# Optimization experiments

Measured on AMD Instinct MI355X. Metric: run time of the kernel, lower is better.

Reference implementation:

```python
import jax, jax.numpy as jnp
import numpy as np

N = 16383        # complete binary tree, 14 levels
D_NODE = 512
D_SSM = 512
D_STATE = 16
MAX_DEPTH = 14   # number of BFS levels (depth 0..13)
LN_EPS = 1e-5


def setup_inputs() -> dict:
    key = jax.random.key(0)
    ks = jax.random.split(key, 8)
    # tree structure: parent[i] = (i-1)//2, root has parent -1; BFS order == index order
    parent = np.concatenate([np.array([-1]), (np.arange(1, N) - 1) // 2]).astype(np.int64)
    depth = np.floor(np.log2(np.arange(N) + 1)).astype(np.int32)
    s = jax.random.normal(ks[0], (N, D_NODE), jnp.float32)
    w = jax.random.uniform(ks[1], (N,), jnp.float32, minval=0.01, maxval=1.0)
    # parameters (xavier-ish scales)
    W_in = jax.random.normal(ks[2], (D_SSM, D_NODE + 1), jnp.float32) * (1.0 / np.sqrt(D_NODE + 1))
    b_in = jnp.zeros((D_SSM,), jnp.float32)
    W_delta = jax.random.normal(ks[3], (D_SSM, D_SSM), jnp.float32) * (1.0 / np.sqrt(D_SSM))
    # dt-style bias init: softplus(b) ~ dt in [1e-3, 1e-1]
    dt = jnp.exp(jax.random.uniform(ks[4], (D_SSM,), jnp.float32) * (np.log(0.1) - np.log(0.001)) + np.log(0.001))
    b_delta = dt + jnp.log(-jnp.expm1(-dt))
    W_w = jax.random.normal(ks[5], (D_SSM, 1), jnp.float32)
    b_w = jnp.zeros((D_SSM,), jnp.float32)
    A_log = jnp.log(jnp.broadcast_to(jnp.arange(1.0, D_STATE + 1.0, dtype=jnp.float32)[None, :], (D_SSM, D_STATE)))
    D = jnp.ones((D_SSM,), jnp.float32)
    W_B = jax.random.normal(ks[6], (D_STATE, D_SSM), jnp.float32) * (1.0 / np.sqrt(D_SSM))
    b_B = jnp.zeros((D_STATE,), jnp.float32)
    W_C = jax.random.normal(ks[7], (D_STATE, D_SSM), jnp.float32) * (1.0 / np.sqrt(D_SSM))
    b_C = jnp.zeros((D_STATE,), jnp.float32)
    gamma = jnp.ones((D_SSM,), jnp.float32)
    beta = jnp.zeros((D_SSM,), jnp.float32)
    return {"s": s, "w": w, "parent": jnp.asarray(parent), "depth": jnp.asarray(depth),
            "W_in": W_in, "b_in": b_in, "W_delta": W_delta, "b_delta": b_delta,
            "W_w": W_w, "b_w": b_w, "A_log": A_log, "D": D,
            "W_B": W_B, "b_B": b_B, "W_C": W_C, "b_C": b_C,
            "gamma": gamma, "beta": beta}


def reference(s, w, parent, depth, W_in, b_in, W_delta, b_delta, W_w, b_w,
              A_log, D, W_B, b_B, W_C, b_C, gamma, beta):
    n = s.shape[0]
    log_w = jnp.log(w + 1e-6)[:, None]                       # [N, 1]
    feat = jnp.concatenate([s, log_w], axis=1)               # [N, d_node+1]
    x = feat @ W_in.T + b_in                                 # [N, d_ssm]
    delta = jax.nn.softplus(x @ W_delta.T + b_delta) * jax.nn.sigmoid(log_w @ W_w.T + b_w)  # [N, d_ssm]
    A = -jnp.exp(A_log)                                      # [d_ssm, d_state]
    B = x @ W_B.T + b_B                                      # [N, d_state]
    C = x @ W_C.T + b_C                                      # [N, d_state]
    A_bar = jnp.exp(delta[:, :, None] * A[None])             # [N, d_ssm, d_state]
    Bx = (delta * x)[:, :, None] * B[:, None, :]             # [N, d_ssm, d_state]
    # level-parallel tree scan: all nodes at BFS depth l updated together
    par = jnp.maximum(parent, 0)
    has_par = (parent >= 0)[:, None, None]
    H = jnp.zeros((n, A_bar.shape[1], A_bar.shape[2]), x.dtype)
    for lvl in range(MAX_DEPTH):
        h_par = jnp.where(has_par, jnp.take(H, par, axis=0), 0.0)
        H = jnp.where((depth == lvl)[:, None, None], A_bar * h_par + Bx, H)
    Y = jnp.einsum('nds,ns->nd', H, C) + D * x               # [N, d_ssm]
    mu = jnp.mean(Y, axis=-1, keepdims=True)
    var = jnp.var(Y, axis=-1, keepdims=True)
    return (Y - mu) / jnp.sqrt(var + LN_EPS) * gamma + beta
```

## Files before the change

### kernel.cpp

```cpp
#include <hip/hip_runtime.h>
#include <hip/hip_bf16.h>
#include <math.h>

#define D_SSM 512
#define D_STATE 16
#define CKPT_BASE 511
#define N_CKPT 512
#define MPAD 16384

typedef __attribute__((ext_vector_type(8))) short short8;
typedef __attribute__((ext_vector_type(4))) float floatx4;

__device__ __forceinline__ unsigned short f2bf(float f) {
    unsigned int u = __float_as_uint(f);
    unsigned int r = (u + 0x7fffu + ((u >> 16) & 1u)) >> 16;
    return (unsigned short)r;
}
__device__ __forceinline__ float bf2f(unsigned short u) {
    return __uint_as_float(((unsigned int)u) << 16);
}
__device__ __forceinline__ void g2lds16(const void* g, void* l) {
    __builtin_amdgcn_global_load_lds(
        (const __attribute__((address_space(1))) void*)g,
        (__attribute__((address_space(3))) void*)l, 16, 0, 0);
}

__device__ __forceinline__ void pw_powers(float r, float* p) {
    float r2 = r * r, r4 = r2 * r2, r8 = r4 * r4;
    p[0] = r;          p[1] = r2;         p[2] = r2 * r;     p[3] = r4;
    p[4] = r4 * r;     p[5] = r4 * r2;    p[6] = r4 * p[2];  p[7] = r8;
    p[8] = r8 * r;     p[9] = r8 * r2;    p[10] = r8 * p[2]; p[11] = r8 * r4;
    p[12] = r8 * p[4]; p[13] = r8 * p[5]; p[14] = r8 * p[6]; p[15] = r8 * r8;
}

__global__ __launch_bounds__(256) void prep_kernel(
    const float* __restrict__ s, const float* __restrict__ w,
    const float* __restrict__ W_in, const float* __restrict__ W_delta,
    const float* __restrict__ W_B, const float* __restrict__ W_C,
    const float* __restrict__ A_log,
    unsigned short* __restrict__ s_bf, float* __restrict__ lw,
    unsigned short* __restrict__ Win_bf, unsigned short* __restrict__ Wd_bf,
    float* __restrict__ As_tab, int* __restrict__ fast_tab,
    int Nn)
{
    const int b = blockIdx.x, t = threadIdx.x;
    if (b < MPAD) {
        unsigned int pack = 0;
        if (b < Nn) {
            float2 sv = *(const float2*)(s + (size_t)b * 512 + t * 2);
            pack = (unsigned int)f2bf(sv.x) | ((unsigned int)f2bf(sv.y) << 16);
        }
        *(unsigned int*)(s_bf + (size_t)b * 512 + t * 2) = pack;
        if (t == 0) lw[b] = (b < Nn) ? logf(w[b] + 1e-6f) : 0.f;
    } else if (b < MPAD + 512) {
        int c = b - MPAD;
        float a0 = W_in[(size_t)c * 513 + t * 2];
        float a1 = W_in[(size_t)c * 513 + t * 2 + 1];
        *(unsigned int*)(Win_bf + (size_t)c * 512 + t * 2) =
            (unsigned int)f2bf(a0) | ((unsigned int)f2bf(a1) << 16);
    } else if (b < MPAD + 1024) {
        int c = b - MPAD - 512;
        float2 wv = *(const float2*)(W_delta + (size_t)c * 512 + t * 2);
        *(unsigned int*)(Wd_bf + (size_t)c * 512 + t * 2) =
            (unsigned int)f2bf(wv.x) | ((unsigned int)f2bf(wv.y) << 16);
    } else if (b < MPAD + 1024 + 128) {
        int c = b - MPAD - 1024;
        float2 wv; wv.x = 0.f; wv.y = 0.f;
        if (c < 16)      wv = *(const float2*)(W_B + (size_t)c * 512 + t * 2);
        else if (c < 32) wv = *(const float2*)(W_C + (size_t)(c - 16) * 512 + t * 2);
        *(unsigned int*)(Wd_bf + (size_t)(512 + c) * 512 + t * 2) =
            (unsigned int)f2bf(wv.x) | ((unsigned int)f2bf(wv.y) << 16);
    } else {
        int ch = (b - (MPAD + 1024 + 128)) * 256 + t;
        float As0 = -__expf(A_log[ch * 16]);
        bool ok = true;
        #pragma unroll
        for (int q = 1; q < 16; q++) {
            float As = -__expf(A_log[ch * 16 + q]);
            ok = ok && (fabsf(As - (float)(q + 1) * As0) <= 1e-4f * (float)(q + 1));
        }
        As_tab[ch] = As0;
        fast_tab[ch] = ok ? 1 : 0;
    }
}

__global__ __launch_bounds__(256) void gemm_mfma(
    const unsigned short* __restrict__ Abf,
    const unsigned short* __restrict__ Wbf,
    float* __restrict__ outf,
    unsigned short* __restrict__ outbf,
    const float* __restrict__ bias,
    const float* __restrict__ lw,
    const float* __restrict__ wcol, int wcol_stride,
    const float* __restrict__ bw,
    const float* __restrict__ b_B, const float* __restrict__ b_C,
    float* __restrict__ Bm, float* __restrict__ Cm,
    int mode)
{
    __shared__ __align__(16) short As[2][128 * 32];
    __shared__ __align__(16) short Bs[2][128 * 32];
    const int tid = threadIdx.x;
    const int wave = tid >> 6, lane = tid & 63;

    const int nwg  = gridDim.x * gridDim.y;
    const int orig = blockIdx.y * gridDim.x + blockIdx.x;
    const int wsw  = (orig & 7) * (nwg >> 3) + (orig >> 3);
    const int bx   = wsw % gridDim.x;
    const int by   = wsw / gridDim.x;
    const int row0 = by * 128;
    const int col0 = bx * 128;

    const int wr = (wave >> 1) * 64;
    const int wc = (wave & 1) * 64;

    floatx4 acc[4][4] = {};

    const int srow = lane >> 2;
    const int sg   = (lane & 3) ^ ((srow >> 1) & 3);
    const int scol = sg * 8;

    const unsigned short* Ag = Abf + (size_t)(row0 + wave * 16 + srow) * 512 + scol;
    const unsigned short* Wg = Wbf + (size_t)(col0 + wave * 16 + srow) * 512 + scol;
    char* Al = (char*)&As[0][0] + wave * 1024;
    char* Bl = (char*)&Bs[0][0] + wave * 1024;

    #define STAGE(buf, k0)                                              \
        do {                                                            \
            g2lds16(Ag + (k0),            Al + (buf) * 8192);           \
            g2lds16(Ag + 64 * 512 + (k0), Al + (buf) * 8192 + 4096);    \
            g2lds16(Wg + (k0),            Bl + (buf) * 8192);           \
            g2lds16(Wg + 64 * 512 + (k0), Bl + (buf) * 8192 + 4096);    \
        } while (0)

    STAGE(0, 0);
    __syncthreads();

    for (int it = 0; it < 16; ++it) {
        const int cur = it & 1;
        if (it < 15) STAGE(cur ^ 1, (it + 1) * 32);

        short8 af[4], bfr[4];
        #pragma unroll
        for (int i = 0; i < 4; i++) {
            int m = wr + i * 16 + (lane & 15);
            int gm = (lane >> 4) ^ ((m >> 1) & 3);
            af[i] = *(const short8*)&As[cur][m * 32 + gm * 8];
        }
        #pragma unroll
        for (int j = 0; j < 4; j++) {
            int n = wc + j * 16 + (lane & 15);
            int gn = (lane >> 4) ^ ((n >> 1) & 3);
            bfr[j] = *(const short8*)&Bs[cur][n * 32 + gn * 8];
        }
        #pragma unroll
        for (int i = 0; i < 4; i++)
            #pragma unroll
            for (int j = 0; j < 4; j++)
                acc[i][j] = __builtin_amdgcn_mfma_f32_16x16x32_bf16(af[i], bfr[j], acc[i][j], 0, 0, 0);
        __syncthreads();
    }
    #undef STAGE

    if (col0 >= 512) {
        #pragma unroll
        for (int i = 0; i < 4; i++) {
            #pragma unroll
            for (int reg = 0; reg < 4; reg++) {
                int r = row0 + wr + i * 16 + (lane >> 4) * 4 + reg;
                #pragma unroll
                for (int j = 0; j < 4; j++) {
                    int c2 = wc + j * 16 + (lane & 15);
                    float z = acc[i][j][reg];
                    if (c2 < 16)      Bm[(size_t)r * 16 + c2]        = z + b_B[c2];
                    else if (c2 < 32) Cm[(size_t)r * 16 + (c2 - 16)] = z + b_C[c2 - 16];
                }
            }
        }
        return;
    }

    #pragma unroll
    for (int i = 0; i < 4; i++) {
        #pragma unroll
        for (int reg = 0; reg < 4; reg++) {
            int r = row0 + wr + i * 16 + (lane >> 4) * 4 + reg;
            float lwr = lw[r];
            #pragma unroll
            for (int j = 0; j < 4; j++) {
                int c = col0 + wc + j * 16 + (lane & 15);
                float z = acc[i][j][reg] + bias[c];
                if (mode == 0) {
                    float o = z + lwr * wcol[(size_t)c * wcol_stride];
                    outbf[(size_t)r * 512 + c] = f2bf(o);
                } else {
                    float sp = (z > 15.f) ? z : __logf(1.f + __expf(z));
                    float sg2 = __builtin_amdgcn_rcpf(1.f + __expf(-(lwr * wcol[c] + bw[c])));
                    outf[(size_t)r * 512 + c] = sp * sg2;
                }
            }
        }
    }
}

__global__ __launch_bounds__(512, 4) void scan_fused(
    const unsigned short* __restrict__ x_bf, const float* __restrict__ delta,
    const float* __restrict__ Bm, const float* __restrict__ Cm,
    const float* __restrict__ A_log, const float* __restrict__ Dv,
    const float* __restrict__ gamma, const float* __restrict__ beta,
    const float* __restrict__ As_tab, const int* __restrict__ fast_tab,
    float* __restrict__ out)
{
    __shared__ __align__(16) float SMEM[16 * 512 + 31 * 32 + 10 * 16];
    __shared__ int nid[16];
    const int bid = blockIdx.x;
    const int d = threadIdx.x;

    const float As0 = As_tab[d];
    const bool fast = fast_tab[d] != 0;
    const float dvd = Dv[d];

    if (bid < N_CKPT) {
        const int a9 = CKPT_BASE + bid;
        float* const Yb   = SMEM;
        float* const BCs  = SMEM + 8192;
        float* const Banc = SMEM + 8192 + 992;

        for (int idx = d; idx < 31 * 32; idx += 512) {
            int i = idx >> 5, c = idx & 31;
            int v = i + 1;
            int j = 31 - __builtin_clz((unsigned)v);
            int node = ((a9 + 1) << j) - 1 + (v - (1 << j));
            BCs[i * 32 + c] = (c < 16) ? Bm[(size_t)node * 16 + c]
                                       : Cm[(size_t)node * 16 + (c - 16)];
        }
        if (d < 160) {
            int k = d >> 4, ss = d & 15;
            int a = a9;
            for (int q = 0; q < k; q++) a = (a - 1) >> 1;
            Banc[k * 16 + ss] = Bm[(size_t)a * 16 + ss];
        }

        float adl[10]; unsigned short axr[10];
        {
            int a = a9;
            #pragma unroll
            for (int k = 0; k < 10; k++) {
                adl[k] = delta[(size_t)a * 512 + d];
                axr[k] = x_bf[(size_t)a * 512 + d];
                a = (a - 1) >> 1;
            }
        }

        const int n10a = 2 * a9 + 1, n10b = 2 * a9 + 2;
        float pdl[2][7]; unsigned short pxr[2][7]; int pid[2][7];
        auto pf7 = [&](int n11, float* dl, unsigned short* xr, int* id) {
            id[0] = n11;          id[1] = 2 * n11 + 1; id[2] = 2 * id[1] + 1;
            id[3] = id[2] + 1;    id[4] = 2 * n11 + 2; id[5] = 2 * id[4] + 1;
            id[6] = id[5] + 1;
            #pragma unroll
            for (int q = 0; q < 7; q++) {
                dl[q] = delta[(size_t)id[q] * 512 + d];
                xr[q] = x_bf[(size_t)id[q] * 512 + d];
            }
        };
        float d10a = delta[(size_t)n10a * 512 + d];
        unsigned short x10a = x_bf[(size_t)n10a * 512 + d];
        pf7(2 * n10a + 1, pdl[0], pxr[0], pid[0]);

        __syncthreads();

        float H9v[16];
        #pragma unroll
        for (int ss = 0; ss < 16; ss++) H9v[ss] = 0.f;
        {
            float cum = 0.f;
            #pragma unroll
            for (int k = 0; k < 10; k++) {
                float da = adl[k];
                float bx = da * bf2f(axr[k]);
                if (fast) {
                    float r = __expf(As0 * cum);
                    float pw[16]; pw_powers(r, pw);
                    const floatx4* B4 = (const floatx4*)&Banc[k * 16];
                    #pragma unroll
                    for (int q = 0; q < 4; q++) {
                        floatx4 b = B4[q];
                        #pragma unroll
                        for (int u = 0; u < 4; u++) {
                            int ss = q * 4 + u;
                            H9v[ss] = fmaf(bx * pw[ss], b[u], H9v[ss]);
                        }
                    }
                } else {
                    #pragma unroll
                    for (int ss = 0; ss < 16; ss++) {
                        float As = -__expf(A_log[d * 16 + ss]);
                        H9v[ss] = fmaf(bx * __expf(As * cum), Banc[k * 16 + ss], H9v[ss]);
                    }
                }
                cum += da;
            }
        }

        auto step_pf = [&](int bfs, float dlt, unsigned short xraw,
                           const float* Hp, float* Hc, int slot, int n) {
            float xv = bf2f(xraw);
            float bx = dlt * xv;
            float y0 = 0.f, y1 = 0.f;
            const floatx4* B4 = (const floatx4*)&BCs[bfs * 32];
            const floatx4* C4 = (const floatx4*)&BCs[bfs * 32 + 16];
            if (fast) {
                float r = __expf(As0 * dlt);
                float pw[16]; pw_powers(r, pw);
                #pragma unroll
                for (int q = 0; q < 4; q++) {
                    floatx4 b = B4[q], c = C4[q];
                    #pragma unroll
                    for (int u = 0; u < 4; u++) {
                        int ss = q * 4 + u;
                        Hc[ss] = fmaf(pw[ss], Hp[ss], bx * b[u]);
                        if (ss & 1) y1 = fmaf(c[u], Hc[ss], y1);
                        else        y0 = fmaf(c[u], Hc[ss], y0);
                    }
                }
            } else {
                #pragma unroll
                for (int ss = 0; ss < 16; ss++) {
                    float Ab = __expf(dlt * (-__expf(A_log[d * 16 + ss])));
                    Hc[ss] = fmaf(Ab, Hp[ss], bx * BCs[bfs * 32 + ss]);
                    float cc = BCs[bfs * 32 + 16 + ss];
                    if (ss & 1) y1 = fmaf(cc, Hc[ss], y1);
                    else        y0 = fmaf(cc, Hc[ss], y0);
                }
            }
            Yb[slot * 512 + d] = fmaf(dvd, xv, y0 + y1);
            if (d == 0) nid[slot] = n;
        };
        auto leaf_pf = [&](int bfs, float dlt, unsigned short xraw,
                           const float* Hp, int slot, int n) {
            float xv = bf2f(xraw);
            float bx = dlt * xv;
            float y0 = 0.f, y1 = 0.f;
            const floatx4* B4 = (const floatx4*)&BCs[bfs * 32];
            const floatx4* C4 = (const floatx4*)&BCs[bfs * 32 + 16];
            if (fast) {
                float r = __expf(As0 * dlt);
                float pw[16]; pw_powers(r, pw);
                #pragma unroll
                for (int q = 0; q < 4; q++) {
                    floatx4 b = B4[q], c = C4[q];
                    #pragma unroll
                    for (int u = 0; u < 4; u++) {
                        int ss = q * 4 + u;
                        float h = fmaf(pw[ss], Hp[ss], bx * b[u]);
                        if (ss & 1) y1 = fmaf(c[u], h, y1);
                        else        y0 = fmaf(c[u], h, y0);
                    }
                }
            } else {
                #pragma unroll
                for (int ss = 0; ss < 16; ss++) {
                    float Ab = __expf(dlt * (-__expf(A_log[d * 16 + ss])));
                    float h = fmaf(Ab, Hp[ss], bx * BCs[bfs * 32 + ss]);
                    float cc = BCs[bfs * 32 + 16 + ss];
                    if (ss & 1) y1 = fmaf(cc, h, y1);
                    else        y0 = fmaf(cc, h, y0);
                }
            }
            Yb[slot * 512 + d] = fmaf(dvd, xv, y0 + y1);
            if (d == 0) nid[slot] = n;
        };
        auto flush = [&](int cnt) {
            const int w = d >> 6, lane = d & 63;
            for (int i = w; i < cnt; i += 8) {
                int n = nid[i];
                float v[8]; float s1 = 0.f, s2 = 0.f;
                #pragma unroll
                for (int k = 0; k < 8; k++) {
                    v[k] = Yb[i * 512 + lane + 64 * k];
                    s1 += v[k]; s2 += v[k] * v[k];
                }
                #pragma unroll
                for (int off = 32; off > 0; off >>= 1) {
                    s1 += __shfl_xor(s1, off);
                    s2 += __shfl_xor(s2, off);
                }
                float mu = s1 * (1.f / 512.f);
                float inv = rsqrtf(s2 * (1.f / 512.f) - mu * mu + 1e-5f);
                #pragma unroll
                for (int k = 0; k < 8; k++) {
                    int ch = lane + 64 * k;
                    out[(size_t)n * 512 + ch] = (v[k] - mu) * inv * gamma[ch] + beta[ch];
                }
            }
        };

        {
            float xv = bf2f(axr[0]);
            const floatx4* C4 = (const floatx4*)&BCs[16];
            float y0 = 0.f, y1 = 0.f;
            #pragma unroll
            for (int q = 0; q < 4; q++) {
                floatx4 c = C4[q];
                #pragma unroll
                for (int u = 0; u < 4; u++) {
                    int ss = q * 4 + u;
                    if (ss & 1) y1 = fmaf(c[u], H9v[ss], y1);
                    else        y0 = fmaf(c[u], H9v[ss], y0);
                }
            }
            Yb[d] = fmaf(dvd, xv, y0 + y1);
            if (d == 0) nid[0] = a9;
        }

        float H10[16], H11[16], H12[16];
        float d10b; unsigned short x10b;

        step_pf(1, d10a, x10a, H9v, H10, 1, n10a);
        pf7(2 * n10a + 2, pdl[1], pxr[1], pid[1]);
        step_pf(3,  pdl[0][0], pxr[0][0], H10, H11, 2, pid[0][0]);
        step_pf(7,  pdl[0][1], pxr[0][1], H11, H12, 3, pid[0][1]);
        leaf_pf(15, pdl[0][2], pxr[0][2], H12, 4, pid[0][2]);
        leaf_pf(16, pdl[0][3], pxr[0][3], H12, 5, pid[0][3]);
        step_pf(8,  pdl[0][4], pxr[0][4], H11, H12, 6, pid[0][4]);
        leaf_pf(17, pdl[0][5], pxr[0][5], H12, 7, pid[0][5]);
        leaf_pf(18, pdl[0][6], pxr[0][6], H12, 8, pid[0][6]);
        d10b = delta[(size_t)n10b * 512 + d];
        x10b = x_bf[(size_t)n10b * 512 + d];
        pf7(2 * n10b + 1, pdl[0], pxr[0], pid[0]);
        step_pf(4,  pdl[1][0], pxr[1][0], H10, H11, 9,  pid[1][0]);
        step_pf(9,  pdl[1][1], pxr[1][1], H11, H12, 10, pid[1][1]);
        leaf_pf(19, pdl[1][2], pxr[1][2], H12, 11, pid[1][2]);
        leaf_pf(20, pdl[1][3], pxr[1][3], H12, 12, pid[1][3]);
        step_pf(10, pdl[1][4], pxr[1][4], H11, H12, 13, pid[1][4]);
        leaf_pf(21, pdl[1][5], pxr[1][5], H12, 14, pid[1][5]);
        leaf_pf(22, pdl[1][6], pxr[1][6], H12, 15, pid[1][6]);
        __syncthreads();
        flush(16);
        __syncthreads();

        step_pf(2, d10b, x10b, H9v, H10, 0, n10b);
        pf7(2 * n10b + 2, pdl[1], pxr[1], pid[1]);
        step_pf(5,  pdl[0][0], pxr[0][0], H10, H11, 1, pid[0][0]);
        step_pf(11, pdl[0][1], pxr[0][1], H11, H12, 2, pid[0][1]);
        leaf_pf(23, pdl[0][2], pxr[0][2], H12, 3, pid[0][2]);
        leaf_pf(24, pdl[0][3], pxr[0][3], H12, 4, pid[0][3]);
        step_pf(12, pdl[0][4], pxr[0][4], H11, H12, 5, pid[0][4]);
        leaf_pf(25, pdl[0][5], pxr[0][5], H12, 6, pid[0][5]);
        leaf_pf(26, pdl[0][6], pxr[0][6], H12, 7, pid[0][6]);
        step_pf(6,  pdl[1][0], pxr[1][0], H10, H11, 8,  pid[1][0]);
        step_pf(13, pdl[1][1], pxr[1][1], H11, H12, 9,  pid[1][1]);
        leaf_pf(27, pdl[1][2], pxr[1][2], H12, 10, pid[1][2]);
        leaf_pf(28, pdl[1][3], pxr[1][3], H12, 11, pid[1][3]);
        step_pf(14, pdl[1][4], pxr[1][4], H11, H12, 12, pid[1][4]);
        leaf_pf(29, pdl[1][5], pxr[1][5], H12, 13, pid[1][5]);
        leaf_pf(30, pdl[1][6], pxr[1][6], H12, 14, pid[1][6]);
        __syncthreads();
        flush(15);
    } else {
        const int n = bid - N_CKPT;
        float* const Banc9 = SMEM;
        float* const Cn    = SMEM + 144;
        float* const red   = SMEM + 160;

        if (d < 144) {
            int k = d >> 4, ss = d & 15;
            int a = n;
            for (int q = 0; q < 9; q++) if (q < k) a = (a < 0) ? -1 : ((a - 1) >> 1);
            Banc9[k * 16 + ss] = (a >= 0) ? Bm[(size_t)a * 16 + ss] : 0.f;
        }
        if (d >= 240 && d < 256) Cn[d - 240] = Cm[(size_t)n * 16 + (d - 240)];

        float adl[9]; unsigned short axr[9];
        {
            int a = n;
            #pragma unroll
            for (int k = 0; k < 9; k++) {
                bool v = a >= 0;
                adl[k] = v ? delta[(size_t)a * 512 + d] : 0.f;
                axr[k] = v ? x_bf[(size_t)a * 512 + d] : (unsigned short)0;
                a = v ? ((a - 1) >> 1) : -1;
            }
        }
        __syncthreads();

        float acc[16];
        #pragma unroll
        for (int ss = 0; ss < 16; ss++) acc[ss] = 0.f;

        float cum = 0.f;
        #pragma unroll
        for (int k = 0; k < 9; k++) {
            float da = adl[k];
            float bx = da * bf2f(axr[k]);
            if (fast) {
                float r = __expf(As0 * cum);
                float pw[16]; pw_powers(r, pw);
                const floatx4* B4 = (const floatx4*)&Banc9[k * 16];
                #pragma unroll
                for (int q = 0; q < 4; q++) {
                    floatx4 b = B4[q];
                    #pragma unroll
                    for (int u = 0; u < 4; u++) {
                        int ss = q * 4 + u;
                        acc[ss] = fmaf(bx * pw[ss], b[u], acc[ss]);
                    }
                }
            } else {
                #pragma unroll
                for (int ss = 0; ss < 16; ss++) {
                    float As = -__expf(A_log[d * 16 + ss]);
                    acc[ss] = fmaf(bx * __expf(As * cum), Banc9[k * 16 + ss], acc[ss]);
                }
            }
            cum += da;
        }

        float xv = bf2f(axr[0]);
        float y0 = 0.f, y1 = 0.f;
        const floatx4* C4 = (const floatx4*)&Cn[0];
        #pragma unroll
        for (int q = 0; q < 4; q++) {
            floatx4 c = C4[q];
            #pragma unroll
            for (int u = 0; u < 4; u++) {
                int ss = q * 4 + u;
                if (ss & 1) y1 = fmaf(c[u], acc[ss], y1);
                else        y0 = fmaf(c[u], acc[ss], y0);
            }
        }
        float y = fmaf(dvd, xv, y0 + y1);

        float s1 = y, s2 = y * y;
        #pragma unroll
        for (int off = 32; off > 0; off >>= 1) {
            s1 += __shfl_xor(s1, off);
            s2 += __shfl_xor(s2, off);
        }
        int wid = d >> 6, lane = d & 63;
        if (lane == 0) { red[wid] = s1; red[wid + 8] = s2; }
        __syncthreads();
        float S1 = 0.f, S2 = 0.f;
        #pragma unroll
        for (int k = 0; k < 8; k++) { S1 += red[k]; S2 += red[k + 8]; }
        float mu = S1 * (1.f / 512.f);
        float var = S2 * (1.f / 512.f) - mu * mu;
        float inv = rsqrtf(var + 1e-5f);
        out[(size_t)n * 512 + d] = (y - mu) * inv * gamma[d] + beta[d];
    }
}

extern "C" void kernel_launch(void* const* d_in, const int* in_sizes, int n_in,
                              void* d_out, int out_size, void* d_ws, size_t ws_size,
                              hipStream_t stream) {
    const float* s_in   = (const float*)d_in[0];
    const float* w      = (const float*)d_in[1];
    const float* W_in    = (const float*)d_in[4];
    const float* b_in    = (const float*)d_in[5];
    const float* W_delta = (const float*)d_in[6];
    const float* b_delta = (const float*)d_in[7];
    const float* W_w     = (const float*)d_in[8];
    const float* b_w     = (const float*)d_in[9];
    const float* A_log   = (const float*)d_in[10];
    const float* Dv      = (const float*)d_in[11];
    const float* W_B     = (const float*)d_in[12];
    const float* b_B     = (const float*)d_in[13];
    const float* W_C     = (const float*)d_in[14];
    const float* b_C     = (const float*)d_in[15];
    const float* gamma   = (const float*)d_in[16];
    const float* beta    = (const float*)d_in[17];
    float* out = (float*)d_out;

    const int Nn = in_sizes[1];

    float* ws    = (float*)d_ws;
    float* lw    = ws;
    float* delta = lw + MPAD;
    float* Bm    = delta + (size_t)MPAD * 512;
    float* Cm    = Bm + (size_t)MPAD * 16;
    unsigned short* s_bf  = (unsigned short*)(Cm + (size_t)MPAD * 16);
    unsigned short* x_bf  = s_bf + (size_t)MPAD * 512;
    unsigned short* Win_bf = x_bf + (size_t)MPAD * 512;
    unsigned short* Wd_bf  = Win_bf + 512 * 512;
    float* As_tab  = (float*)(Wd_bf + 640 * 512);
    int*   fast_tab = (int*)(As_tab + 512);

    prep_kernel<<<MPAD + 1024 + 128 + 2, 256, 0, stream>>>(
        s_in, w, W_in, W_delta, W_B, W_C, A_log,
        s_bf, lw, Win_bf, Wd_bf, As_tab, fast_tab, Nn);

    dim3 g1(4, 128);
    gemm_mfma<<<g1, 256, 0, stream>>>(s_bf, Win_bf, nullptr, x_bf,
                                      b_in, lw, W_in + 512, 513, nullptr,
                                      nullptr, nullptr, nullptr, nullptr, 0);
    dim3 g2(5, 128);
    gemm_mfma<<<g2, 256, 0, stream>>>(x_bf, Wd_bf, delta, nullptr,
                                      b_delta, lw, W_w, 1, b_w,
                                      b_B, b_C, Bm, Cm, 1);

    scan_fused<<<N_CKPT + CKPT_BASE, 512, 0, stream>>>(
        x_bf, delta, Bm, Cm, A_log, Dv, gamma, beta, As_tab, fast_tab, out);
}
```

Before: 234.1 us.

## Split ancestor prefetch into two halves and relax scan launch bounds

The ancestor delta/x loads for the checkpoint H9 reconstruction are now done in two batches of five instead of ten at once. The second batch is issued only after the first half of the accumulation, which cuts live registers. The root-node x value is reloaded from global memory instead of kept in a register. Launch bounds drop from 4 to 2 blocks per CU, giving the compiler more registers per thread at the possible cost of occupancy, and the split exposes load latency mid-computation.

```diff
diff --git a/kernel.cpp b/kernel.cpp
--- a/kernel.cpp
+++ b/kernel.cpp
@@ -202,7 +202,7 @@
     }
 }
 
-__global__ __launch_bounds__(512, 4) void scan_fused(
+__global__ __launch_bounds__(512, 2) void scan_fused(
     const unsigned short* __restrict__ x_bf, const float* __restrict__ delta,
     const float* __restrict__ Bm, const float* __restrict__ Cm,
     const float* __restrict__ A_log, const float* __restrict__ Dv,
@@ -240,15 +240,17 @@
             Banc[k * 16 + ss] = Bm[(size_t)a * 16 + ss];
         }
 
-        float adl[10]; unsigned short axr[10];
+        float adl[5]; unsigned short axr[5];
+        int anc5;
         {
             int a = a9;
             #pragma unroll
-            for (int k = 0; k < 10; k++) {
+            for (int k = 0; k < 5; k++) {
                 adl[k] = delta[(size_t)a * 512 + d];
                 axr[k] = x_bf[(size_t)a * 512 + d];
                 a = (a - 1) >> 1;
             }
+            anc5 = a;
         }
 
         const int n10a = 2 * a9 + 1, n10b = 2 * a9 + 2;
@@ -272,34 +274,67 @@
         float H9v[16];
         #pragma unroll
         for (int ss = 0; ss < 16; ss++) H9v[ss] = 0.f;
+        float cum = 0.f;
+        #pragma unroll
+        for (int k = 0; k < 5; k++) {
+            float da = adl[k];
+            float bx = da * bf2f(axr[k]);
+            if (fast) {
+                float r = __expf(As0 * cum);
+                float pw[16]; pw_powers(r, pw);
+                const floatx4* B4 = (const floatx4*)&Banc[k * 16];
+                #pragma unroll
+                for (int q = 0; q < 4; q++) {
+                    floatx4 b = B4[q];
+                    #pragma unroll
+                    for (int u = 0; u < 4; u++) {
+                        int ss = q * 4 + u;
+                        H9v[ss] = fmaf(bx * pw[ss], b[u], H9v[ss]);
+                    }
+                }
+            } else {
+                #pragma unroll
+                for (int ss = 0; ss < 16; ss++) {
+                    float As = -__expf(A_log[d * 16 + ss]);
+                    H9v[ss] = fmaf(bx * __expf(As * cum), Banc[k * 16 + ss], H9v[ss]);
+                }
+            }
+            cum += da;
+        }
         {
-            float cum = 0.f;
-            #pragma unroll
-            for (int k = 0; k < 10; k++) {
-                float da = adl[k];
-                float bx = da * bf2f(axr[k]);
-                if (fast) {
-                    float r = __expf(As0 * cum);
-                    float pw[16]; pw_powers(r, pw);
-                    const floatx4* B4 = (const floatx4*)&Banc[k * 16];
+            int a = anc5;
+            #pragma unroll
+            for (int k = 0; k < 5; k++) {
+                adl[k] = delta[(size_t)a * 512 + d];
+                axr[k] = x_bf[(size_t)a * 512 + d];
+                a = (a - 1) >> 1;
+            }
+        }
+        #pragma unroll
+        for (int k = 0; k < 5; k++) {
+            float da = adl[k];
+            float bx = da * bf2f(axr[k]);
+            if (fast) {
+                float r = __expf(As0 * cum);
+                float pw[16]; pw_powers(r, pw);
+                const floatx4* B4 = (const floatx4*)&Banc[(k + 5) * 16];
+                #pragma unroll
+                for (int q = 0; q < 4; q++) {
+                    floatx4 b = B4[q];
                     #pragma unroll
-                    for (int q = 0; q < 4; q++) {
-                        floatx4 b = B4[q];
-                        #pragma unroll
-                        for (int u = 0; u < 4; u++) {
-                            int ss = q * 4 + u;
-                            H9v[ss] = fmaf(bx * pw[ss], b[u], H9v[ss]);
-                        }
+                    for (int u = 0; u < 4; u++) {
+                        int ss = q * 4 + u;
+                        H9v[ss] = fmaf(bx * pw[ss], b[u], H9v[ss]);
                     }
-                } else {
-                    #pragma unroll
-                    for (int ss = 0; ss < 16; ss++) {
-                        float As = -__expf(A_log[d * 16 + ss]);
-                        H9v[ss] = fmaf(bx * __expf(As * cum), Banc[k * 16 + ss], H9v[ss]);
-                    }
-                }
-                cum += da;
-            }
+                }
+            } else {
+                #pragma unroll
+                for (int ss = 0; ss < 16; ss++) {
+                    float As = -__expf(A_log[d * 16 + ss]);
+                    H9v[ss] = fmaf(bx * __expf(As * cum), Banc[(k + 5) * 16 + ss], H9v[ss]);
+                }
+            }
+            cum += da;
         }
 
         auto step_pf = [&](int bfs, float dlt, unsigned short xraw,
@@ -396,7 +431,7 @@
         };
 
         {
-            float xv = bf2f(axr[0]);
+            float xv = bf2f(x_bf[(size_t)a9 * 512 + d]);
             const floatx4* C4 = (const floatx4*)&BCs[16];
             float y0 = 0.f, y1 = 0.f;
             #pragma unroll
```

New measurement: 229.8 us. No clear change (-1.8%).

## Split each depth-9 subtree scan across two blocks, one per child subtree

Applied to the files above, without the earlier changes.

Each checkpoint block previously handled both child subtrees of a depth-9 node sequentially, with manual register prefetch of delta/x. Now twice as many blocks each handle one child subtree, recomputing the shared ancestor state H9, which doubles parallelism and shortens each block's critical path. The manual prefetch pipeline is removed in favour of plain loads, and the occupancy hint in launch_bounds is dropped. This costs redundant ancestor loads and compute, and may raise register pressure or expose more load latency.

```diff
diff --git a/kernel.cpp b/kernel.cpp
--- a/kernel.cpp
+++ b/kernel.cpp
@@ -202,7 +202,7 @@
     }
 }
 
-__global__ __launch_bounds__(512, 4) void scan_fused(
+__global__ __launch_bounds__(512) void scan_fused(
     const unsigned short* __restrict__ x_bf, const float* __restrict__ delta,
     const float* __restrict__ Bm, const float* __restrict__ Cm,
     const float* __restrict__ A_log, const float* __restrict__ Dv,
@@ -219,8 +219,10 @@
     const bool fast = fast_tab[d] != 0;
     const float dvd = Dv[d];
 
-    if (bid < N_CKPT) {
-        const int a9 = CKPT_BASE + bid;
+    if (bid < 2 * N_CKPT) {
+        const int p  = bid & 511;
+        const int c0 = bid >> 9;
+        const int a9 = CKPT_BASE + p;
         float* const Yb   = SMEM;
         float* const BCs  = SMEM + 8192;
         float* const Banc = SMEM + 8192 + 992;
@@ -239,34 +241,6 @@
             for (int q = 0; q < k; q++) a = (a - 1) >> 1;
             Banc[k * 16 + ss] = Bm[(size_t)a * 16 + ss];
         }
-
-        float adl[10]; unsigned short axr[10];
-        {
-            int a = a9;
-            #pragma unroll
-            for (int k = 0; k < 10; k++) {
-                adl[k] = delta[(size_t)a * 512 + d];
-                axr[k] = x_bf[(size_t)a * 512 + d];
-                a = (a - 1) >> 1;
-            }
-        }
-
-        const int n10a = 2 * a9 + 1, n10b = 2 * a9 + 2;
-        float pdl[2][7]; unsigned short pxr[2][7]; int pid[2][7];
-        auto pf7 = [&](int n11, float* dl, unsigned short* xr, int* id) {
-            id[0] = n11;          id[1] = 2 * n11 + 1; id[2] = 2 * id[1] + 1;
-            id[3] = id[2] + 1;    id[4] = 2 * n11 + 2; id[5] = 2 * id[4] + 1;
-            id[6] = id[5] + 1;
-            #pragma unroll
-            for (int q = 0; q < 7; q++) {
-                dl[q] = delta[(size_t)id[q] * 512 + d];
-                xr[q] = x_bf[(size_t)id[q] * 512 + d];
-            }
-        };
-        float d10a = delta[(size_t)n10a * 512 + d];
-        unsigned short x10a = x_bf[(size_t)n10a * 512 + d];
-        pf7(2 * n10a + 1, pdl[0], pxr[0], pid[0]);
-
         __syncthreads();
 
         float H9v[16];
@@ -274,10 +248,11 @@
         for (int ss = 0; ss < 16; ss++) H9v[ss] = 0.f;
         {
             float cum = 0.f;
+            int a = a9;
             #pragma unroll
             for (int k = 0; k < 10; k++) {
-                float da = adl[k];
-                float bx = da * bf2f(axr[k]);
+                float da = delta[(size_t)a * 512 + d];
+                float bx = da * bf2f(x_bf[(size_t)a * 512 + d]);
                 if (fast) {
                     float r = __expf(As0 * cum);
                     float pw[16]; pw_powers(r, pw);
@@ -299,16 +274,17 @@
                     }
                 }
                 cum += da;
-            }
-        }
-
-        auto step_pf = [&](int bfs, float dlt, unsigned short xraw,
-                           const float* Hp, float* Hc, int slot, int n) {
-            float xv = bf2f(xraw);
+                a = (a - 1) >> 1;
+            }
+        }
+
+        auto step = [&](int n, int bfs, const float* Hp, float* Hc, int slot) {
+            float dlt = delta[(size_t)n * 512 + d];
+            float xv = bf2f(x_bf[(size_t)n * 512 + d]);
             float bx = dlt * xv;
-            float y0 = 0.f, y1 = 0.f;
             const floatx4* B4 = (const floatx4*)&BCs[bfs * 32];
             const floatx4* C4 = (const floatx4*)&BCs[bfs * 32 + 16];
+            float y0 = 0.f, y1 = 0.f;
             if (fast) {
                 float r = __expf(As0 * dlt);
                 float pw[16]; pw_powers(r, pw);
@@ -336,13 +312,13 @@
             Yb[slot * 512 + d] = fmaf(dvd, xv, y0 + y1);
             if (d == 0) nid[slot] = n;
         };
-        auto leaf_pf = [&](int bfs, float dlt, unsigned short xraw,
-                           const float* Hp, int slot, int n) {
-            float xv = bf2f(xraw);
+        auto leaf = [&](int n, int bfs, const float* Hp, int slot) {
+            float dlt = delta[(size_t)n * 512 + d];
+            float xv = bf2f(x_bf[(size_t)n * 512 + d]);
             float bx = dlt * xv;
-            float y0 = 0.f, y1 = 0.f;
             const floatx4* B4 = (const floatx4*)&BCs[bfs * 32];
             const floatx4* C4 = (const floatx4*)&BCs[bfs * 32 + 16];
+            float y0 = 0.f, y1 = 0.f;
             if (fast) {
                 float r = __expf(As0 * dlt);
                 float pw[16]; pw_powers(r, pw);
@@ -370,33 +346,10 @@
             Yb[slot * 512 + d] = fmaf(dvd, xv, y0 + y1);
             if (d == 0) nid[slot] = n;
         };
-        auto flush = [&](int cnt) {
-            const int w = d >> 6, lane = d & 63;
-            for (int i = w; i < cnt; i += 8) {
-                int n = nid[i];
-                float v[8]; float s1 = 0.f, s2 = 0.f;
-                #pragma unroll
-                for (int k = 0; k < 8; k++) {
-                    v[k] = Yb[i * 512 + lane + 64 * k];
-                    s1 += v[k]; s2 += v[k] * v[k];
-                }
-                #pragma unroll
-                for (int off = 32; off > 0; off >>= 1) {
-                    s1 += __shfl_xor(s1, off);
-                    s2 += __shfl_xor(s2, off);
-                }
-                float mu = s1 * (1.f / 512.f);
-                float inv = rsqrtf(s2 * (1.f / 512.f) - mu * mu + 1e-5f);
-                #pragma unroll
-                for (int k = 0; k < 8; k++) {
-                    int ch = lane + 64 * k;
-                    out[(size_t)n * 512 + ch] = (v[k] - mu) * inv * gamma[ch] + beta[ch];
-                }
-            }
-        };
-
-        {
-            float xv = bf2f(axr[0]);
+
+        int slot = 0;
+        if (c0 == 0) {
+            float xv = bf2f(x_bf[(size_t)a9 * 512 + d]);
             const floatx4* C4 = (const floatx4*)&BCs[16];
             float y0 = 0.f, y1 = 0.f;
             #pragma unroll
@@ -411,54 +364,54 @@
             }
             Yb[d] = fmaf(dvd, xv, y0 + y1);
             if (d == 0) nid[0] = a9;
+            slot = 1;
         }
 
         float H10[16], H11[16], H12[16];
-        float d10b; unsigned short x10b;
-
-        step_pf(1, d10a, x10a, H9v, H10, 1, n10a);
-        pf7(2 * n10a + 2, pdl[1], pxr[1], pid[1]);
-        step_pf(3,  pdl[0][0], pxr[0][0], H10, H11, 2, pid[0][0]);
-        step_pf(7,  pdl[0][1], pxr[0][1], H11, H12, 3, pid[0][1]);
-        leaf_pf(15, pdl[0][2], pxr[0][2], H12, 4, pid[0][2]);
-        leaf_pf(16, pdl[0][3], pxr[0][3], H12, 5, pid[0][3]);
-        step_pf(8,  pdl[0][4], pxr[0][4], H11, H12, 6, pid[0][4]);
-        leaf_pf(17, pdl[0][5], pxr[0][5], H12, 7, pid[0][5]);
-        leaf_pf(18, pdl[0][6], pxr[0][6], H12, 8, pid[0][6]);
-        d10b = delta[(size_t)n10b * 512 + d];
-        x10b = x_bf[(size_t)n10b * 512 + d];
-        pf7(2 * n10b + 1, pdl[0], pxr[0], pid[0]);
-        step_pf(4,  pdl[1][0], pxr[1][0], H10, H11, 9,  pid[1][0]);
-        step_pf(9,  pdl[1][1], pxr[1][1], H11, H12, 10, pid[1][1]);
-        leaf_pf(19, pdl[1][2], pxr[1][2], H12, 11, pid[1][2]);
-        leaf_pf(20, pdl[1][3], pxr[1][3], H12, 12, pid[1][3]);
-        step_pf(10, pdl[1][4], pxr[1][4], H11, H12, 13, pid[1][4]);
-        leaf_pf(21, pdl[1][5], pxr[1][5], H12, 14, pid[1][5]);
-        leaf_pf(22, pdl[1][6], pxr[1][6], H12, 15, pid[1][6]);
+        const int n10 = 2 * a9 + 1 + c0;
+        step(n10, 1 + c0, H9v, H10, slot++);
+        #pragma unroll
+        for (int c1 = 0; c1 < 2; c1++) {
+            int n11 = 2 * n10 + 1 + c1;
+            step(n11, 3 + 2 * c0 + c1, H10, H11, slot++);
+            #pragma unroll
+            for (int c2 = 0; c2 < 2; c2++) {
+                int n12 = 2 * n11 + 1 + c2;
+                step(n12, 7 + 4 * c0 + 2 * c1 + c2, H11, H12, slot++);
+                #pragma unroll
+                for (int c3 = 0; c3 < 2; c3++) {
+                    int n13 = 2 * n12 + 1 + c3;
+                    leaf(n13, 15 + 8 * c0 + 4 * c1 + 2 * c2 + c3, H12, slot++);
+                }
+            }
+        }
         __syncthreads();
-        flush(16);
-        __syncthreads();
-
-        step_pf(2, d10b, x10b, H9v, H10, 0, n10b);
-        pf7(2 * n10b + 2, pdl[1], pxr[1], pid[1]);
-        step_pf(5,  pdl[0][0], pxr[0][0], H10, H11, 1, pid[0][0]);
-        step_pf(11, pdl[0][1], pxr[0][1], H11, H12, 2, pid[0][1]);
-        leaf_pf(23, pdl[0][2], pxr[0][2], H12, 3, pid[0][2]);
-        leaf_pf(24, pdl[0][3], pxr[0][3], H12, 4, pid[0][3]);
-        step_pf(12, pdl[0][4], pxr[0][4], H11, H12, 5, pid[0][4]);
-        leaf_pf(25, pdl[0][5], pxr[0][5], H12, 6, pid[0][5]);
-        leaf_pf(26, pdl[0][6], pxr[0][6], H12, 7, pid[0][6]);
-        step_pf(6,  pdl[1][0], pxr[1][0], H10, H11, 8,  pid[1][0]);
-        step_pf(13, pdl[1][1], pxr[1][1], H11, H12, 9,  pid[1][1]);
-        leaf_pf(27, pdl[1][2], pxr[1][2], H12, 10, pid[1][2]);
-        leaf_pf(28, pdl[1][3], pxr[1][3], H12, 11, pid[1][3]);
-        step_pf(14, pdl[1][4], pxr[1][4], H11, H12, 12, pid[1][4]);
-        leaf_pf(29, pdl[1][5], pxr[1][5], H12, 13, pid[1][5]);
-        leaf_pf(30, pdl[1][6], pxr[1][6], H12, 14, pid[1][6]);
-        __syncthreads();
-        flush(15);
+
+        const int cnt = (c0 == 0) ? 16 : 15;
+        const int w = d >> 6, lane = d & 63;
+        for (int i = w; i < cnt; i += 8) {
+            int n = nid[i];
+            float v[8]; float s1 = 0.f, s2 = 0.f;
+            #pragma unroll
+            for (int k = 0; k < 8; k++) {
+                v[k] = Yb[i * 512 + lane + 64 * k];
+                s1 += v[k]; s2 += v[k] * v[k];
+            }
+            #pragma unroll
+            for (int off = 32; off > 0; off >>= 1) {
+                s1 += __shfl_xor(s1, off);
+                s2 += __shfl_xor(s2, off);
+            }
+            float mu = s1 * (1.f / 512.f);
+            float inv = rsqrtf(s2 * (1.f / 512.f) - mu * mu + 1e-5f);
+            #pragma unroll
+            for (int k = 0; k < 8; k++) {
+                int ch = lane + 64 * k;
+                out[(size_t)n * 512 + ch] = (v[k] - mu) * inv * gamma[ch] + beta[ch];
+            }
+        }
     } else {
-        const int n = bid - N_CKPT;
+        const int n = bid - 2 * N_CKPT;
         float* const Banc9 = SMEM;
         float* const Cn    = SMEM + 144;
         float* const red   = SMEM + 160;
@@ -598,6 +551,6 @@
                                       b_delta, lw, W_w, 1, b_w,
                                       b_B, b_C, Bm, Cm, 1);
 
-    scan_fused<<<N_CKPT + CKPT_BASE, 512, 0, stream>>>(
+    scan_fused<<<2 * N_CKPT + CKPT_BASE, 512, 0, stream>>>(
         x_bf, delta, Bm, Cm, A_log, Dv, gamma, beta, As_tab, fast_tab, out);
 }
```

New measurement: 218.6 us. 6.6% less time.
